# Kernel tuning notes

Measured on AMD Instinct MI355X. Metric: run time of the kernel, lower is better.

The kernel has to match this reference:

```python
import jax, jax.numpy as jnp
import numpy as np

FP8_MAX = 448.0  # max representable magnitude in float8_e4m3fn
EPS = 1e-12


def setup_inputs() -> dict:
    key = jax.random.key(0)
    k1, k2, k3 = jax.random.split(key, 3)
    B, S, DIN, DOUT = 8, 4096, 1024, 1024
    x = jax.random.normal(k1, (B, S, DIN), dtype=jnp.float32)
    weight = jax.random.normal(k2, (DOUT, DIN), dtype=jnp.float32) * (1.0 / np.sqrt(DIN))
    bias = jax.random.normal(k3, (DOUT,), dtype=jnp.float32) * 0.01
    return {"x": x, "weight": weight, "bias": bias}


def _quantize_fp8(t):
    # per-tensor dynamic scale: amax / 448, clamped
    scale = jnp.maximum(jnp.max(jnp.abs(t)) / FP8_MAX, EPS).astype(jnp.float32)
    t_fp8 = (t / scale).astype(jnp.float8_e4m3fn)
    return t_fp8, scale


def reference(x, weight, bias):
    in_features = weight.shape[1]
    out_features = weight.shape[0]
    # quantize weights (mirrors quantize_weights())
    w_fp8, w_scale = _quantize_fp8(weight)
    # dynamic activation quantization
    x_flat = x.reshape(-1, in_features)  # [M, K]
    x_fp8, x_scale = _quantize_fp8(x_flat)
    # scaled fp8 GEMM: accumulate in fp32, apply per-tensor scales (torch._scaled_mm)
    out = jnp.einsum(
        "mk,nk->mn",
        x_fp8.astype(jnp.float32),
        w_fp8.astype(jnp.float32),
    ) * (x_scale * w_scale)
    out = out.reshape(*x.shape[:-1], out_features)
    return out + bias
```

## Files before the change

kernel.cpp:

```cpp
#include <hip/hip_runtime.h>
#include <cstdint>
#include <cstddef>

typedef float f32x4 __attribute__((ext_vector_type(4)));
typedef long  lx2   __attribute__((ext_vector_type(2)));

#define PXB 1024
#define PWB 64
#define QXB 2048
#define QWB 128

__device__ __forceinline__ void async_copy16(const uint8_t* g, uint8_t* s) {
    __builtin_amdgcn_global_load_lds(
        (const __attribute__((address_space(1))) void*)g,
        (__attribute__((address_space(3))) void*)s,
        16 , 0 , 0 );
}

__device__ __forceinline__ float block_max(float m, float* scr) {
#pragma unroll
    for (int o = 32; o > 0; o >>= 1) m = fmaxf(m, __shfl_down(m, o, 64));
    const int lane = threadIdx.x & 63, wid = threadIdx.x >> 6;
    if (lane == 0) scr[wid] = m;
    __syncthreads();
    const int nw = blockDim.x >> 6;
    m = scr[0];
    for (int j = 1; j < nw; ++j) m = fmaxf(m, scr[j]);
    return m;
}

__global__ void amax_partials(const float4* __restrict__ x, int nx4,
                              const float4* __restrict__ w, int nw4,
                              float* __restrict__ part) {
    __shared__ float scr[8];
    const int b = blockIdx.x;
    const float4* p;
    int n4, nb, bi;
    if (b < PXB) { p = x; n4 = nx4; nb = PXB; bi = b; }
    else         { p = w; n4 = nw4; nb = PWB; bi = b - PXB; }
    float m = 0.0f;
    for (int i = bi * blockDim.x + threadIdx.x; i < n4; i += nb * blockDim.x) {
        float4 v = p[i];
        m = fmaxf(m, fmaxf(fmaxf(fabsf(v.x), fabsf(v.y)),
                           fmaxf(fabsf(v.z), fabsf(v.w))));
    }
    m = block_max(m, scr);
    if (threadIdx.x == 0) part[b] = m;
}

__global__ void quant_fused(const float4* __restrict__ x, int nx16,
                            const float4* __restrict__ w, int nw16,
                            const float* __restrict__ part,
                            int4* __restrict__ xq, int4* __restrict__ wq) {
    __shared__ float scr[8];
    const int b = blockIdx.x;
    const float4* in;
    const float* pp;
    int4* out;
    int n16, nb, bi, np;
    if (b < QXB) { in = x; n16 = nx16; nb = QXB; bi = b;       pp = part;       np = PXB; out = xq; }
    else         { in = w; n16 = nw16; nb = QWB; bi = b - QXB; pp = part + PXB; np = PWB; out = wq; }

    float m = 0.0f;
    for (int i = threadIdx.x; i < np; i += blockDim.x) m = fmaxf(m, pp[i]);
    m = block_max(m, scr);
    const float r = 1.0f / fmaxf(m / 448.0f, 1e-12f);

    for (int i = bi * blockDim.x + threadIdx.x; i < n16; i += nb * blockDim.x) {
        int4 o;
#pragma unroll
        for (int j = 0; j < 4; ++j) {
            float4 v = in[i * 4 + j];
            int p = 0;
            p = __builtin_amdgcn_cvt_pk_fp8_f32(v.x * r, v.y * r, p, false);
            p = __builtin_amdgcn_cvt_pk_fp8_f32(v.z * r, v.w * r, p, true);
            ((int*)&o)[j] = p;
        }
        out[i] = o;
    }
}

__global__ __launch_bounds__(256) void gemm_fp8_kernel(
    const uint8_t* __restrict__ A,
    const uint8_t* __restrict__ B,
    const float* __restrict__ bias,
    const float* __restrict__ part,
    float* __restrict__ out,
    int M, int N, int K) {
    __shared__ long lds64[2048];
    uint8_t* Abase = (uint8_t*)lds64;
    uint8_t* Bbase = Abase + 8192;

    const int tid  = threadIdx.x;
    const int l    = tid & 63;
    const int w    = tid >> 6;
    const int lm   = l & 15;
    const int quad = l >> 4;
    const int wm   = (w >> 1) * 64;
    const int wn   = (w & 1) * 64;

    const size_t am0 = (size_t)blockIdx.y * 128;
    const size_t bn0 = (size_t)blockIdx.x * 128;

    float* scr = (float*)lds64;
    float mx = 0.0f, mw = 0.0f;
    for (int i = tid; i < PXB; i += 256) mx = fmaxf(mx, part[i]);
    for (int i = tid; i < PWB; i += 256) mw = fmaxf(mw, part[PXB + i]);
    mx = block_max(mx, scr);
    mw = block_max(mw, scr + 8);
    const float scale = fmaxf(mx / 448.0f, 1e-12f) * fmaxf(mw / 448.0f, 1e-12f);
    __syncthreads();

    f32x4 acc[4][4];
#pragma unroll
    for (int i = 0; i < 4; ++i)
#pragma unroll
        for (int j = 0; j < 4; ++j) acc[i][j] = (f32x4)0.0f;

    const int slot0 = w * 64 + l;

    for (int kt = 0; kt < K; kt += 64) {
#pragma unroll
        for (int i = 0; i < 2; ++i) {
            const int s    = i * 256 + slot0;
            const int row  = s >> 2;
            const int chnk = s & 3;
            async_copy16(A + (am0 + row) * K + kt + chnk * 16,
                         Abase + (i * 4 + w) * 1024);
            async_copy16(B + (bn0 + row) * K + kt + chnk * 16,
                         Bbase + (i * 4 + w) * 1024);
        }
        __syncthreads();

        lx2 a[4], b[4];
#pragma unroll
        for (int t = 0; t < 4; ++t) {
            a[t] = *(const lx2*)&lds64[(wm + t * 16 + lm) * 8 + quad * 2];
            b[t] = *(const lx2*)&lds64[1024 + (wn + t * 16 + lm) * 8 + quad * 2];
        }
#pragma unroll
        for (int ks = 0; ks < 2; ++ks)
#pragma unroll
            for (int mt = 0; mt < 4; ++mt)
#pragma unroll
                for (int nt = 0; nt < 4; ++nt)
                    acc[mt][nt] = __builtin_amdgcn_mfma_f32_16x16x32_fp8_fp8(
                        a[mt][ks], b[nt][ks], acc[mt][nt], 0, 0, 0);
        __syncthreads();
    }

#pragma unroll
    for (int nt = 0; nt < 4; ++nt) {
        const int n = (int)bn0 + wn + nt * 16 + lm;
        const float bv = bias[n];
#pragma unroll
        for (int mt = 0; mt < 4; ++mt) {
            const size_t mrow = am0 + wm + mt * 16 + quad * 4;
#pragma unroll
            for (int r = 0; r < 4; ++r) {
                out[(mrow + r) * (size_t)N + n] = acc[mt][nt][r] * scale + bv;
            }
        }
    }
}

extern "C" void kernel_launch(void* const* d_in, const int* in_sizes, int n_in,
                              void* d_out, int out_size, void* d_ws,
                              size_t ws_size, hipStream_t stream) {
    const float* x      = (const float*)d_in[0];
    const float* weight = (const float*)d_in[1];
    const float* bias   = (const float*)d_in[2];
    float* out          = (float*)d_out;

    const int nx = in_sizes[0];
    const int nw = in_sizes[1];
    const int N  = in_sizes[2];
    const int K  = nw / N;
    const int M  = nx / K;

    float* part     = (float*)d_ws;
    uint8_t* x_fp8  = (uint8_t*)d_ws + 8192;
    uint8_t* w_fp8  = x_fp8 + (size_t)nx;

    amax_partials<<<PXB + PWB, 256, 0, stream>>>(
        (const float4*)x, nx / 4, (const float4*)weight, nw / 4, part);
    quant_fused<<<QXB + QWB, 256, 0, stream>>>(
        (const float4*)x, nx / 16, (const float4*)weight, nw / 16, part,
        (int4*)x_fp8, (int4*)w_fp8);
    gemm_fp8_kernel<<<dim3(N / 128, M / 128), 256, 0, stream>>>(
        x_fp8, w_fp8, bias, part, out, M, N, K);
}
```

Measured before the change: 318.4 us.

## Unroll amax/quant with fixed chunks per block and XCD-aware GEMM tile mapping

The amax and quantize kernels drop their grid-stride loops. Each block now handles a fixed contiguous 16K-float chunk with 16 unrolled coalesced float4 loads, which puts more loads in flight. The GEMM switches to a 1D grid whose block-to-tile mapping gives each of the 8 XCDs a contiguous band of M rows, so the x_fp8 tiles are reused within that XCD's L2. The new code hardcodes M=32768 and N=1024 (32 row tiles per XCD, 8 column tiles) and sizes that divide exactly, so it breaks for other shapes.

```diff
diff --git a/kernel.cpp b/kernel.cpp
--- a/kernel.cpp
+++ b/kernel.cpp
@@ -5,10 +5,8 @@
 typedef float f32x4 __attribute__((ext_vector_type(4)));
 typedef long  lx2   __attribute__((ext_vector_type(2)));
 
-#define PXB 1024
-#define PWB 64
-#define QXB 2048
-#define QWB 128
+#define AXB 2048
+#define AWB 64
 
 __device__ __forceinline__ void async_copy16(const uint8_t* g, uint8_t* s) {
     __builtin_amdgcn_global_load_lds(
@@ -29,54 +27,61 @@
     return m;
 }
 
-__global__ void amax_partials(const float4* __restrict__ x, int nx4,
-                              const float4* __restrict__ w, int nw4,
+__global__ void amax_partials(const float4* __restrict__ x,
+                              const float4* __restrict__ w,
                               float* __restrict__ part) {
     __shared__ float scr[8];
     const int b = blockIdx.x;
     const float4* p;
-    int n4, nb, bi;
-    if (b < PXB) { p = x; n4 = nx4; nb = PXB; bi = b; }
-    else         { p = w; n4 = nw4; nb = PWB; bi = b - PXB; }
-    float m = 0.0f;
-    for (int i = bi * blockDim.x + threadIdx.x; i < n4; i += nb * blockDim.x) {
-        float4 v = p[i];
-        m = fmaxf(m, fmaxf(fmaxf(fabsf(v.x), fabsf(v.y)),
-                           fmaxf(fabsf(v.z), fabsf(v.w))));
-    }
-    m = block_max(m, scr);
-    if (threadIdx.x == 0) part[b] = m;
-}
-
-__global__ void quant_fused(const float4* __restrict__ x, int nx16,
-                            const float4* __restrict__ w, int nw16,
+    int bi;
+    if (b < AXB) { p = x; bi = b; }
+    else         { p = w; bi = b - AXB; }
+    const float4* base = p + (size_t)bi * 4096 + threadIdx.x;
+
+    float m[16];
+#pragma unroll
+    for (int u = 0; u < 16; ++u) {
+        float4 v = base[u * 256];
+        m[u] = fmaxf(fmaxf(fabsf(v.x), fabsf(v.y)),
+                     fmaxf(fabsf(v.z), fabsf(v.w)));
+    }
+#pragma unroll
+    for (int s = 8; s > 0; s >>= 1)
+#pragma unroll
+        for (int u = 0; u < s; ++u) m[u] = fmaxf(m[u], m[u + s]);
+
+    float r = block_max(m[0], scr);
+    if (threadIdx.x == 0) part[b] = r;
+}
+
+__global__ void quant_fused(const float4* __restrict__ x,
+                            const float4* __restrict__ w,
                             const float* __restrict__ part,
-                            int4* __restrict__ xq, int4* __restrict__ wq) {
+                            unsigned* __restrict__ xq,
+                            unsigned* __restrict__ wq) {
     __shared__ float scr[8];
     const int b = blockIdx.x;
     const float4* in;
     const float* pp;
-    int4* out;
-    int n16, nb, bi, np;
-    if (b < QXB) { in = x; n16 = nx16; nb = QXB; bi = b;       pp = part;       np = PXB; out = xq; }
-    else         { in = w; n16 = nw16; nb = QWB; bi = b - QXB; pp = part + PXB; np = PWB; out = wq; }
+    unsigned* out;
+    int bi, np;
+    if (b < AXB) { in = x; bi = b;       pp = part;       np = AXB; out = xq; }
+    else         { in = w; bi = b - AXB; pp = part + AXB; np = AWB; out = wq; }
 
     float m = 0.0f;
     for (int i = threadIdx.x; i < np; i += blockDim.x) m = fmaxf(m, pp[i]);
     m = block_max(m, scr);
     const float r = 1.0f / fmaxf(m / 448.0f, 1e-12f);
 
-    for (int i = bi * blockDim.x + threadIdx.x; i < n16; i += nb * blockDim.x) {
-        int4 o;
-#pragma unroll
-        for (int j = 0; j < 4; ++j) {
-            float4 v = in[i * 4 + j];
-            int p = 0;
-            p = __builtin_amdgcn_cvt_pk_fp8_f32(v.x * r, v.y * r, p, false);
-            p = __builtin_amdgcn_cvt_pk_fp8_f32(v.z * r, v.w * r, p, true);
-            ((int*)&o)[j] = p;
-        }
-        out[i] = o;
+    const float4* base = in + (size_t)bi * 4096 + threadIdx.x;
+    unsigned* obase = out + (size_t)bi * 4096 + threadIdx.x;
+#pragma unroll
+    for (int u = 0; u < 16; ++u) {
+        float4 v = base[u * 256];
+        int p = 0;
+        p = __builtin_amdgcn_cvt_pk_fp8_f32(v.x * r, v.y * r, p, false);
+        p = __builtin_amdgcn_cvt_pk_fp8_f32(v.z * r, v.w * r, p, true);
+        obase[u * 256] = (unsigned)p;
     }
 }
 
@@ -99,13 +104,16 @@
     const int wm   = (w >> 1) * 64;
     const int wn   = (w & 1) * 64;
 
-    const size_t am0 = (size_t)blockIdx.y * 128;
-    const size_t bn0 = (size_t)blockIdx.x * 128;
+    const int b     = blockIdx.x;
+    const int xcd   = b & 7;
+    const int local = b >> 3;
+    const size_t am0 = ((size_t)xcd * 32 + (local >> 3)) * 128;
+    const size_t bn0 = (size_t)(local & 7) * 128;
 
     float* scr = (float*)lds64;
     float mx = 0.0f, mw = 0.0f;
-    for (int i = tid; i < PXB; i += 256) mx = fmaxf(mx, part[i]);
-    for (int i = tid; i < PWB; i += 256) mw = fmaxf(mw, part[PXB + i]);
+    for (int i = tid; i < AXB; i += 256) mx = fmaxf(mx, part[i]);
+    for (int i = tid; i < AWB; i += 256) mw = fmaxf(mw, part[AXB + i]);
     mx = block_max(mx, scr);
     mw = block_max(mw, scr + 8);
     const float scale = fmaxf(mx / 448.0f, 1e-12f) * fmaxf(mw / 448.0f, 1e-12f);
@@ -132,11 +140,11 @@
         }
         __syncthreads();
 
-        lx2 a[4], b[4];
+        lx2 a[4], bb[4];
 #pragma unroll
         for (int t = 0; t < 4; ++t) {
-            a[t] = *(const lx2*)&lds64[(wm + t * 16 + lm) * 8 + quad * 2];
-            b[t] = *(const lx2*)&lds64[1024 + (wn + t * 16 + lm) * 8 + quad * 2];
+            a[t]  = *(const lx2*)&lds64[(wm + t * 16 + lm) * 8 + quad * 2];
+            bb[t] = *(const lx2*)&lds64[1024 + (wn + t * 16 + lm) * 8 + quad * 2];
         }
 #pragma unroll
         for (int ks = 0; ks < 2; ++ks)
@@ -145,7 +153,7 @@
 #pragma unroll
                 for (int nt = 0; nt < 4; ++nt)
                     acc[mt][nt] = __builtin_amdgcn_mfma_f32_16x16x32_fp8_fp8(
-                        a[mt][ks], b[nt][ks], acc[mt][nt], 0, 0, 0);
+                        a[mt][ks], bb[nt][ks], acc[mt][nt], 0, 0, 0);
         __syncthreads();
     }
 
@@ -179,14 +187,14 @@
     const int M  = nx / K;
 
     float* part     = (float*)d_ws;
-    uint8_t* x_fp8  = (uint8_t*)d_ws + 8192;
+    uint8_t* x_fp8  = (uint8_t*)d_ws + 16384;
     uint8_t* w_fp8  = x_fp8 + (size_t)nx;
 
-    amax_partials<<<PXB + PWB, 256, 0, stream>>>(
-        (const float4*)x, nx / 4, (const float4*)weight, nw / 4, part);
-    quant_fused<<<QXB + QWB, 256, 0, stream>>>(
-        (const float4*)x, nx / 16, (const float4*)weight, nw / 16, part,
-        (int4*)x_fp8, (int4*)w_fp8);
-    gemm_fp8_kernel<<<dim3(N / 128, M / 128), 256, 0, stream>>>(
+    amax_partials<<<AXB + AWB, 256, 0, stream>>>(
+        (const float4*)x, (const float4*)weight, part);
+    quant_fused<<<AXB + AWB, 256, 0, stream>>>(
+        (const float4*)x, (const float4*)weight, part,
+        (unsigned*)x_fp8, (unsigned*)w_fp8);
+    gemm_fp8_kernel<<<(M / 128) * (N / 128), 256, 0, stream>>>(
         x_fp8, w_fp8, bias, part, out, M, N, K);
 }
```

New measurement: 330.5 us. +3.8%, slower.
